# Kernel tuning notes

Measured on AMD Instinct MI355X. Metric: run time of the kernel, lower is better.

The kernel has to match this reference:

```python
import jax, jax.numpy as jnp
import numpy as np

EMBED_DIM = 1024
N_HEADS = 16
HEAD_DIM = EMBED_DIM // N_HEADS


def setup_inputs() -> dict:
    key = jax.random.key(0)
    ks = jax.random.split(key, 9)
    s = 1.0 / np.sqrt(EMBED_DIM)
    x = jax.random.normal(ks[0], (4, 2048, EMBED_DIM), dtype=jnp.float32)
    Wq = jax.random.uniform(ks[1], (EMBED_DIM, EMBED_DIM), jnp.float32, -s, s)
    bq = jax.random.uniform(ks[2], (EMBED_DIM,), jnp.float32, -s, s)
    Wk = jax.random.uniform(ks[3], (EMBED_DIM, EMBED_DIM), jnp.float32, -s, s)
    bk = jax.random.uniform(ks[4], (EMBED_DIM,), jnp.float32, -s, s)
    Wv = jax.random.uniform(ks[5], (EMBED_DIM, EMBED_DIM), jnp.float32, -s, s)
    bv = jax.random.uniform(ks[6], (EMBED_DIM,), jnp.float32, -s, s)
    Wo = jax.random.uniform(ks[7], (EMBED_DIM, EMBED_DIM), jnp.float32, -s, s)
    bo = jax.random.uniform(ks[8], (EMBED_DIM,), jnp.float32, -s, s)
    return {"x": x, "Wq": Wq, "bq": bq, "Wk": Wk, "bk": bk,
            "Wv": Wv, "bv": bv, "Wo": Wo, "bo": bo}


def reference(x, Wq, bq, Wk, bk, Wv, bv, Wo, bo):
    B, S, _ = x.shape
    # projections (PyTorch Linear: x @ W.T + b; weights stored as [in,out] here)
    q = x @ Wq + bq
    k = x @ Wk + bk
    v = x @ Wv + bv
    # [B, H, S, D]
    q = q.reshape(B, S, N_HEADS, HEAD_DIM).transpose(0, 2, 1, 3)
    k = k.reshape(B, S, N_HEADS, HEAD_DIM).transpose(0, 2, 1, 3)
    v = v.reshape(B, S, N_HEADS, HEAD_DIM).transpose(0, 2, 1, 3)
    scores = jnp.einsum('bhsd,bhtd->bhst', q, k) / np.sqrt(HEAD_DIM).astype(np.float32)
    attn = jax.nn.softmax(scores, axis=-1)
    out = jnp.einsum('bhst,bhtd->bhsd', attn, v)
    out = out.transpose(0, 2, 1, 3).reshape(B, S, EMBED_DIM)
    return out @ Wo + bo  # dropout=0 (eval) -> identity
```

## Files before the change

### kernel.cpp

```cpp
#include <hip/hip_runtime.h>
#include <stdint.h>

#define EMBED 1024
#define NH 16
#define HD 64
#define SEQ 2048
#define BATCH 4
#define M_TOT (BATCH*SEQ)
#define QSCALE 0.18033688011112042f

typedef __attribute__((ext_vector_type(8))) short short8;
typedef __attribute__((ext_vector_type(4))) float floatx4;
typedef __attribute__((ext_vector_type(4))) unsigned int uintx4;

__device__ __forceinline__ unsigned short f2bf(float f) {
    union { float f; unsigned int u; } v; v.f = f;
    unsigned int r = v.u + 0x7fffu + ((v.u >> 16) & 1u);
    return (unsigned short)(r >> 16);
}

__device__ __forceinline__ void load_lds16(const unsigned short* g, unsigned short* l) {
    __builtin_amdgcn_global_load_lds(
        (const __attribute__((address_space(1))) unsigned int*)g,
        (__attribute__((address_space(3))) unsigned int*)l, 16, 0, 0);
}

__global__ void cvt_x(const float* __restrict__ x, unsigned short* __restrict__ xb) {
    int i = (blockIdx.x * 256 + threadIdx.x) * 4;
    float4 v = *(const float4*)(x + i);
    ushort4 o;
    o.x = f2bf(v.x); o.y = f2bf(v.y); o.z = f2bf(v.z); o.w = f2bf(v.w);
    *(ushort4*)(xb + i) = o;
}

__global__ void wtrans(const float* __restrict__ w0, const float* __restrict__ w1,
                       const float* __restrict__ w2, const float* __restrict__ w3,
                       unsigned short* __restrict__ t0, unsigned short* __restrict__ t1,
                       unsigned short* __restrict__ t2, unsigned short* __restrict__ t3) {
    __shared__ float tile[32][33];
    const float* W; unsigned short* T;
    switch (blockIdx.z) { case 0: W=w0; T=t0; break; case 1: W=w1; T=t1; break;
                          case 2: W=w2; T=t2; break; default: W=w3; T=t3; }
    int n0 = blockIdx.x * 32, k0 = blockIdx.y * 32;
    int tx = threadIdx.x, ty = threadIdx.y;
    #pragma unroll
    for (int i = 0; i < 4; i++)
        tile[ty + i*8][tx] = W[(k0 + ty + i*8) * EMBED + n0 + tx];
    __syncthreads();
    #pragma unroll
    for (int i = 0; i < 4; i++)
        T[(n0 + ty + i*8) * EMBED + k0 + tx] = f2bf(tile[tx][ty + i*8]);
}

#define ST32(kt_) do { \
    const int b_ = (kt_) & 3; \
    const unsigned short* sa_ = Asrc + (kt_)*32; \
    const unsigned short* sb_ = Bsrc + (kt_)*32; \
    unsigned short* da_ = ldstA + b_*16384; \
    unsigned short* db_ = ldstB + b_*16384; \
    load_lds16(sa_,             da_); \
    load_lds16(sa_ + 128*EMBED, da_ + 4096); \
    load_lds16(sb_,             db_); \
    load_lds16(sb_ + 128*EMBED, db_ + 4096); \
  } while(0)

template<int WAITN, bool STG>
__device__ __forceinline__ void kt32(int t,
        const unsigned short* Abase, const unsigned short* Bbase,
        const unsigned short* Asrc, const unsigned short* Bsrc,
        unsigned short* ldstA, unsigned short* ldstB, floatx4 (&acc)[8][4]) {
    const int bo = (t & 3) * 16384;
    short8 fA[8], fB[4];
    #pragma unroll
    for (int m=0;m<8;m++) fA[m] = *(const short8*)(Abase + bo + m*512);
    #pragma unroll
    for (int n=0;n<4;n++) fB[n] = *(const short8*)(Bbase + bo + n*512);
    if (STG) ST32(t+3);
    #pragma unroll
    for (int m=0;m<8;m++)
      #pragma unroll
      for (int n=0;n<4;n++)
        acc[m][n] = __builtin_amdgcn_mfma_f32_16x16x32_bf16(fA[m], fB[n], acc[m][n], 0,0,0);
    if (WAITN >= 0) {
        asm volatile("s_waitcnt vmcnt(%0)" :: "i"(WAITN >= 0 ? WAITN : 0) : "memory");
        asm volatile("s_barrier" ::: "memory");
    }
}

template<int MODE>
__global__ __launch_bounds__(512, 2) void gemm32(
        const unsigned short* __restrict__ A, const unsigned short* __restrict__ BT,
        const float* __restrict__ b0, const float* __restrict__ b1, const float* __restrict__ b2,
        void* __restrict__ o0, void* __restrict__ o1, void* __restrict__ o2) {
    __shared__ unsigned short lds[4*16384];
    const int tid = threadIdx.x;
    const int lane = tid & 63, wave = tid >> 6;
    const int quad = lane >> 4, l16 = lane & 15;
    const int wm = wave >> 2, wn = wave & 3;
    const int id = blockIdx.x;
    const int xcd = id & 7, j = id >> 3;
    const int mblk = (xcd * 4 + (j & 3)) * 256;
    const int nblk = (j >> 2) * 256;

    const int srow = tid >> 2;
    const int scol = ((tid & 3) ^ (srow & 3)) * 8;
    const unsigned short* Asrc = A  + (size_t)(mblk + srow) * EMBED + scol;
    const unsigned short* Bsrc = BT + (size_t)(nblk + srow) * EMBED + scol;
    unsigned short* ldstA = lds + wave * 512;
    unsigned short* ldstB = lds + 8192 + wave * 512;

    const int cs = (quad ^ (l16 & 3)) * 8;
    const unsigned short* Abase = lds + (wm*128 + l16)*32 + cs;
    const unsigned short* Bbase = lds + 8192 + (wn*64 + l16)*32 + cs;

    floatx4 acc[8][4];
    #pragma unroll
    for (int m=0;m<8;m++)
      #pragma unroll
      for (int n=0;n<4;n++) acc[m][n] = (floatx4){0.f,0.f,0.f,0.f};

    ST32(0); ST32(1); ST32(2);
    asm volatile("s_waitcnt vmcnt(8)" ::: "memory");
    asm volatile("s_barrier" ::: "memory");

    #pragma unroll 4
    for (int t = 0; t < 28; ++t)
        kt32<8,true>(t, Abase, Bbase, Asrc, Bsrc, ldstA, ldstB, acc);
    kt32<8,true >(28, Abase, Bbase, Asrc, Bsrc, ldstA, ldstB, acc);
    kt32<4,false>(29, Abase, Bbase, Asrc, Bsrc, ldstA, ldstB, acc);
    kt32<0,false>(30, Abase, Bbase, Asrc, Bsrc, ldstA, ldstB, acc);
    kt32<-1,false>(31, Abase, Bbase, Asrc, Bsrc, ldstA, ldstB, acc);

    if (MODE == 1) {
        float* O = (float*)o0;
        #pragma unroll
        for (int mt=0;mt<8;mt++)
          #pragma unroll
          for (int nt=0;nt<4;nt++) {
            int col = nblk + wn*64 + nt*16 + l16;
            float bv = b0[col];
            #pragma unroll
            for (int r=0;r<4;r++) {
                int row = mblk + wm*128 + mt*16 + quad*4 + r;
                O[(size_t)row * EMBED + col] = acc[mt][nt][r] + bv;
            }
          }
    } else {
        int which = nblk >> 10;
        const float* bs = (which==0) ? b0 : (which==1) ? b1 : b2;
        if (which < 2) {
            unsigned short* O = (unsigned short*)((which==0) ? o0 : o1);
            float sc = (which==0) ? QSCALE : 1.f;
            #pragma unroll
            for (int mt=0;mt<8;mt++)
              #pragma unroll
              for (int nt=0;nt<4;nt++) {
                int coll = (nblk & 1023) + wn*64 + nt*16 + l16;
                float bv = bs[coll];
                int h = coll >> 6, d = coll & 63;
                #pragma unroll
                for (int r=0;r<4;r++) {
                    int row = mblk + wm*128 + mt*16 + quad*4 + r;
                    int b = row >> 11, s = row & 2047;
                    O[((size_t)(b*NH + h)*SEQ + s)*HD + d] = f2bf((acc[mt][nt][r] + bv) * sc);
                }
              }
        } else {
            unsigned short* T = lds;
            __syncthreads();
            #pragma unroll
            for (int nt=0;nt<4;nt++) {
                int cloc = wn*64 + nt*16 + l16;
                float bv = bs[(nblk & 1023) + cloc];
                int sw = (cloc & 3) << 3;
                #pragma unroll
                for (int mt=0;mt<8;mt++) {
                    int row0 = wm*128 + mt*16 + quad*4;
                    int sp0 = (row0 & ~31) | (((row0 >> 2) & 3) << 3) | (((row0 >> 4) & 1) << 2);
                    ushort4 w;
                    w.x = f2bf(acc[mt][nt][0] + bv);
                    w.y = f2bf(acc[mt][nt][1] + bv);
                    w.z = f2bf(acc[mt][nt][2] + bv);
                    w.w = f2bf(acc[mt][nt][3] + bv);
                    *(ushort4*)(T + cloc*256 + (sp0 ^ sw)) = w;
                }
            }
            __syncthreads();
            unsigned short* OV = (unsigned short*)o2;
            int s0 = (lane & 31) * 8, dloc = lane >> 5;
            size_t rowbase = ((size_t)((mblk >> 11)*1024 + (nblk & 1023))) * SEQ + (mblk & 2047);
            #pragma unroll
            for (int i=0;i<16;i++) {
                int c = wave*32 + i*2 + dloc;
                int sw2 = (c & 3) << 3;
                short8 v = *(const short8*)(T + c*256 + (s0 ^ sw2));
                *(short8*)(OV + rowbase + (size_t)c * SEQ + s0) = v;
            }
        }
    }
}

__global__ __launch_bounds__(512, 4) void attn(
    const unsigned short* __restrict__ Q, const unsigned short* __restrict__ K,
    const unsigned short* __restrict__ VTp, unsigned short* __restrict__ O) {
    __shared__ unsigned short kv[2][4096];
    unsigned short* kvf = &kv[0][0];
    int tid = threadIdx.x;
    int lane = tid & 63, wave = tid >> 6;
    int quad = lane >> 4, l16 = lane & 15;
    int id = blockIdx.x;
    int bh = (id & 7) * 8 + (id >> 6);
    int qblk = (id >> 3) & 7;
    int b = bh >> 4, h = bh & 15;
    int q0 = qblk * 256 + wave * 32;
    const unsigned short* Qb = Q + (size_t)bh * SEQ * HD;
    const unsigned short* Kb = K + (size_t)bh * SEQ * HD;
    const unsigned short* Vb = VTp + (size_t)bh * HD * SEQ;
    int li = (wave & 3) * 64 + lane;
    const unsigned short* src;
    int dstofs = (wave & 3) * 512 + ((wave >> 2) ? 2048 : 0);
    int src_step;
    if (wave < 4) {
        int t = li >> 3, slot = li & 7;
        int dblk = slot ^ (t & 7);
        src = Kb + (size_t)t * HD + dblk * 8;
        src_step = 32 * HD;
    } else {
        int d = li >> 2, slot = li & 3;
        int swz = (d & 3) ^ ((d >> 2) & 3);
        src = Vb + (size_t)d * SEQ + (slot ^ swz) * 8;
        src_step = 32;
    }
    short8 qf[2][2];
    #pragma unroll
    for (int mt=0;mt<2;mt++) {
        const unsigned short* qp = Qb + (size_t)(q0 + mt*16 + l16) * HD + quad*8;
        qf[mt][0] = *(const short8*)(qp);
        qf[mt][1] = *(const short8*)(qp + 32);
    }
    floatx4 o_acc[2][4], l_acc[2];
    #pragma unroll
    for (int mt=0;mt<2;mt++) {
        l_acc[mt] = (floatx4){0.f,0.f,0.f,0.f};
        #pragma unroll
        for (int dt=0;dt<4;dt++) o_acc[mt][dt] = (floatx4){0.f,0.f,0.f,0.f};
    }
    short8 ones;
    #pragma unroll
    for (int jj=0;jj<8;jj++) ones[jj] = (short)0x3F80;
    int koff[2][2], voff[4];
    #pragma unroll
    for (int nt=0;nt<2;nt++) {
        int t = nt*16 + l16;
        #pragma unroll
        for (int hh=0;hh<2;hh++)
            koff[nt][hh] = t*64 + ((hh*4 + quad) ^ (t & 7)) * 8;
    }
    #pragma unroll
    for (int dt=0;dt<4;dt++) {
        int d = dt*16 + l16;
        voff[dt] = 2048 + d*32 + ((quad ^ (d & 3) ^ ((d >> 2) & 3))) * 8;
    }

    load_lds16(src, kvf + dstofs);
    src += src_step;

    for (int it = 0; it < 64; ++it) {
        const unsigned short* kb = kvf + (it & 1) * 4096;
        if (it < 63) {
            load_lds16(src, kvf + ((it & 1) ^ 1) * 4096 + dstofs);
            src += src_step;
            asm volatile("s_waitcnt vmcnt(1)" ::: "memory");
        } else {
            asm volatile("s_waitcnt vmcnt(0)" ::: "memory");
        }
        __builtin_amdgcn_s_barrier();
        asm volatile("" ::: "memory");
        short8 kf[2][2], vf[4];
        #pragma unroll
        for (int nt=0;nt<2;nt++) {
            kf[nt][0] = *(const short8*)(kb + koff[nt][0]);
            kf[nt][1] = *(const short8*)(kb + koff[nt][1]);
        }
        #pragma unroll
        for (int dt=0;dt<4;dt++)
            vf[dt] = *(const short8*)(kb + voff[dt]);
        floatx4 sacc[2][2];
        __builtin_amdgcn_s_setprio(1);
        #pragma unroll
        for (int nt=0;nt<2;nt++)
          #pragma unroll
          for (int mt=0;mt<2;mt++) {
            floatx4 s = (floatx4){0.f,0.f,0.f,0.f};
            s = __builtin_amdgcn_mfma_f32_16x16x32_bf16(kf[nt][0], qf[mt][0], s, 0, 0, 0);
            s = __builtin_amdgcn_mfma_f32_16x16x32_bf16(kf[nt][1], qf[mt][1], s, 0, 0, 0);
            sacc[nt][mt] = s;
          }
        __builtin_amdgcn_s_setprio(0);
        short8 pf[2];
        #pragma unroll
        for (int mt=0;mt<2;mt++) {
            uintx4 pu;
            #pragma unroll
            for (int jp=0;jp<4;jp++) {
                int nt = jp >> 1, rp = (jp & 1) * 2;
                union { float f; unsigned int u; } e0, e1;
                e0.f = __builtin_amdgcn_exp2f(sacc[nt][mt][rp]);
                e1.f = __builtin_amdgcn_exp2f(sacc[nt][mt][rp+1]);
                pu[jp] = ((e1.u + 0x8000u) & 0xFFFF0000u) | ((e0.u + 0x8000u) >> 16);
            }
            pf[mt] = __builtin_bit_cast(short8, pu);
        }
        __builtin_amdgcn_s_setprio(1);
        #pragma unroll
        for (int mt=0;mt<2;mt++) {
            l_acc[mt] = __builtin_amdgcn_mfma_f32_16x16x32_bf16(ones, pf[mt], l_acc[mt], 0, 0, 0);
            #pragma unroll
            for (int dt=0;dt<4;dt++)
                o_acc[mt][dt] = __builtin_amdgcn_mfma_f32_16x16x32_bf16(vf[dt], pf[mt], o_acc[mt][dt], 0, 0, 0);
        }
        __builtin_amdgcn_s_setprio(0);
        asm volatile("" ::: "memory");
        __builtin_amdgcn_s_barrier();
    }
    #pragma unroll
    for (int mt=0;mt<2;mt++) {
        float inv = 1.f / l_acc[mt][0];
        int s = q0 + mt*16 + l16;
        #pragma unroll
        for (int dt=0;dt<4;dt++) {
            ushort4 w;
            w.x = f2bf(o_acc[mt][dt][0]*inv);
            w.y = f2bf(o_acc[mt][dt][1]*inv);
            w.z = f2bf(o_acc[mt][dt][2]*inv);
            w.w = f2bf(o_acc[mt][dt][3]*inv);
            *(ushort4*)(O + ((size_t)b*SEQ + s)*EMBED + h*HD + dt*16 + quad*4) = w;
        }
    }
}

extern "C" void kernel_launch(void* const* d_in, const int* in_sizes, int n_in,
                              void* d_out, int out_size, void* d_ws, size_t ws_size,
                              hipStream_t stream) {
    const float* x  = (const float*)d_in[0];
    const float* Wq = (const float*)d_in[1]; const float* bq = (const float*)d_in[2];
    const float* Wk = (const float*)d_in[3]; const float* bk = (const float*)d_in[4];
    const float* Wv = (const float*)d_in[5]; const float* bv = (const float*)d_in[6];
    const float* Wo = (const float*)d_in[7]; const float* bo = (const float*)d_in[8];
    char* ws = (char*)d_ws;
    unsigned short* xb  = (unsigned short*)(ws);
    unsigned short* WqT = (unsigned short*)(ws + (16ull<<20));
    unsigned short* WkT = (unsigned short*)(ws + (18ull<<20));
    unsigned short* WvT = (unsigned short*)(ws + (20ull<<20));
    unsigned short* WoT = (unsigned short*)(ws + (22ull<<20));
    unsigned short* Qb  = (unsigned short*)(ws + (24ull<<20));
    unsigned short* Kb  = (unsigned short*)(ws + (40ull<<20));
    unsigned short* VTb = (unsigned short*)(ws + (56ull<<20));
    unsigned short* Ob  = xb;

    cvt_x<<<(M_TOT*EMBED)/1024, 256, 0, stream>>>(x, xb);
    wtrans<<<dim3(32,32,4), dim3(32,8), 0, stream>>>(Wq,Wk,Wv,Wo, WqT,WkT,WvT,WoT);
    gemm32<0><<<dim3(384), 512, 0, stream>>>(xb, WqT, bq, bk, bv, Qb, Kb, VTb);
    attn<<<dim3(512), 512, 0, stream>>>(Qb, Kb, VTb, Ob);
    gemm32<1><<<dim3(128), 512, 0, stream>>>(Ob, WoT, bo, bo, bo, (float*)d_out, nullptr, nullptr);
}
```

Before: 267.7 us.

## Template GEMM on tile shape, switch to double buffering, retile output projection

Replaces the fixed 256x256 GEMM, which used a 4-stage LDS ring with 3-ahead prefetch, with a templated kernel using 2-stage double buffering and a full vmcnt(0) wait each k-step. This roughly halves LDS use so occupancy can rise (launch bound of 4 blocks per CU). The output projection now uses 128x128 tiles with 4 waves across 512 blocks instead of 128 large blocks, to fill the GPU better. The V-transpose epilogue is split into passes so it fits the smaller LDS. The risk is that the shallower prefetch exposes global-load latency, especially in the QKV GEMM, whose tiles are unchanged.

```diff
diff --git a/kernel.cpp b/kernel.cpp
--- a/kernel.cpp
+++ b/kernel.cpp
@@ -52,96 +52,88 @@
         T[(n0 + ty + i*8) * EMBED + k0 + tx] = f2bf(tile[tx][ty + i*8]);
 }
 
-#define ST32(kt_) do { \
-    const int b_ = (kt_) & 3; \
-    const unsigned short* sa_ = Asrc + (kt_)*32; \
-    const unsigned short* sb_ = Bsrc + (kt_)*32; \
-    unsigned short* da_ = ldstA + b_*16384; \
-    unsigned short* db_ = ldstB + b_*16384; \
-    load_lds16(sa_,             da_); \
-    load_lds16(sa_ + 128*EMBED, da_ + 4096); \
-    load_lds16(sb_,             db_); \
-    load_lds16(sb_ + 128*EMBED, db_ + 4096); \
-  } while(0)
-
-template<int WAITN, bool STG>
-__device__ __forceinline__ void kt32(int t,
-        const unsigned short* Abase, const unsigned short* Bbase,
-        const unsigned short* Asrc, const unsigned short* Bsrc,
-        unsigned short* ldstA, unsigned short* ldstB, floatx4 (&acc)[8][4]) {
-    const int bo = (t & 3) * 16384;
-    short8 fA[8], fB[4];
-    #pragma unroll
-    for (int m=0;m<8;m++) fA[m] = *(const short8*)(Abase + bo + m*512);
-    #pragma unroll
-    for (int n=0;n<4;n++) fB[n] = *(const short8*)(Bbase + bo + n*512);
-    if (STG) ST32(t+3);
-    #pragma unroll
-    for (int m=0;m<8;m++)
-      #pragma unroll
-      for (int n=0;n<4;n++)
-        acc[m][n] = __builtin_amdgcn_mfma_f32_16x16x32_bf16(fA[m], fB[n], acc[m][n], 0,0,0);
-    if (WAITN >= 0) {
-        asm volatile("s_waitcnt vmcnt(%0)" :: "i"(WAITN >= 0 ? WAITN : 0) : "memory");
-        asm volatile("s_barrier" ::: "memory");
-    }
-}
-
-template<int MODE>
-__global__ __launch_bounds__(512, 2) void gemm32(
+template<int MODE, int BM, int BN, int NW>
+__global__ __launch_bounds__(NW*64, 4) void gemmk(
         const unsigned short* __restrict__ A, const unsigned short* __restrict__ BT,
         const float* __restrict__ b0, const float* __restrict__ b1, const float* __restrict__ b2,
         void* __restrict__ o0, void* __restrict__ o1, void* __restrict__ o2) {
-    __shared__ unsigned short lds[4*16384];
+    constexpr int THREADS = NW*64;
+    constexpr int WC = NW/2;
+    constexpr int WMT = BM/2, WNT = BN/WC;
+    constexpr int FM = WMT/16, FN = WNT/16;
+    constexpr int RPI = THREADS/4;
+    constexpr int BUFS = (BM+BN)*32;
+    static_assert(BM == 2*RPI && BN == 2*RPI, "staging assumes 2 issues/operand");
+    __shared__ unsigned short lds[2*BUFS];
     const int tid = threadIdx.x;
     const int lane = tid & 63, wave = tid >> 6;
     const int quad = lane >> 4, l16 = lane & 15;
-    const int wm = wave >> 2, wn = wave & 3;
+    const int wm = wave / WC, wn = wave % WC;
     const int id = blockIdx.x;
+    constexpr int MS = (M_TOT/BM)/8;
     const int xcd = id & 7, j = id >> 3;
-    const int mblk = (xcd * 4 + (j & 3)) * 256;
-    const int nblk = (j >> 2) * 256;
+    const int mblk = (xcd * MS + (j % MS)) * BM;
+    const int nblk = (j / MS) * BN;
 
     const int srow = tid >> 2;
     const int scol = ((tid & 3) ^ (srow & 3)) * 8;
     const unsigned short* Asrc = A  + (size_t)(mblk + srow) * EMBED + scol;
     const unsigned short* Bsrc = BT + (size_t)(nblk + srow) * EMBED + scol;
-    unsigned short* ldstA = lds + wave * 512;
-    unsigned short* ldstB = lds + 8192 + wave * 512;
+    unsigned short* sda = lds + wave * 512;
+    unsigned short* sdb = lds + BM*32 + wave * 512;
 
     const int cs = (quad ^ (l16 & 3)) * 8;
-    const unsigned short* Abase = lds + (wm*128 + l16)*32 + cs;
-    const unsigned short* Bbase = lds + 8192 + (wn*64 + l16)*32 + cs;
-
-    floatx4 acc[8][4];
-    #pragma unroll
-    for (int m=0;m<8;m++)
+    const unsigned short* Abase = lds + (wm*WMT + l16)*32 + cs;
+    const unsigned short* Bbase = lds + BM*32 + (wn*WNT + l16)*32 + cs;
+
+    floatx4 acc[FM][FN];
+    #pragma unroll
+    for (int m=0;m<FM;m++)
       #pragma unroll
-      for (int n=0;n<4;n++) acc[m][n] = (floatx4){0.f,0.f,0.f,0.f};
-
-    ST32(0); ST32(1); ST32(2);
-    asm volatile("s_waitcnt vmcnt(8)" ::: "memory");
+      for (int n=0;n<FN;n++) acc[m][n] = (floatx4){0.f,0.f,0.f,0.f};
+
+#define ST(t_) do { \
+    const int buf_ = (t_) & 1; const int ko_ = (t_)*32; \
+    load_lds16(Asrc + ko_,              sda + buf_*BUFS); \
+    load_lds16(Asrc + ko_ + RPI*EMBED,  sda + buf_*BUFS + RPI*32); \
+    load_lds16(Bsrc + ko_,              sdb + buf_*BUFS); \
+    load_lds16(Bsrc + ko_ + RPI*EMBED,  sdb + buf_*BUFS + RPI*32); \
+  } while(0)
+
+    ST(0);
+    asm volatile("s_waitcnt vmcnt(0)" ::: "memory");
     asm volatile("s_barrier" ::: "memory");
 
-    #pragma unroll 4
-    for (int t = 0; t < 28; ++t)
-        kt32<8,true>(t, Abase, Bbase, Asrc, Bsrc, ldstA, ldstB, acc);
-    kt32<8,true >(28, Abase, Bbase, Asrc, Bsrc, ldstA, ldstB, acc);
-    kt32<4,false>(29, Abase, Bbase, Asrc, Bsrc, ldstA, ldstB, acc);
-    kt32<0,false>(30, Abase, Bbase, Asrc, Bsrc, ldstA, ldstB, acc);
-    kt32<-1,false>(31, Abase, Bbase, Asrc, Bsrc, ldstA, ldstB, acc);
-
-    if (MODE == 1) {
+    #pragma unroll 2
+    for (int t = 0; t < 32; ++t) {
+        const int bo = (t & 1) * BUFS;
+        short8 fA[FM], fB[FN];
+        #pragma unroll
+        for (int m=0;m<FM;m++) fA[m] = *(const short8*)(Abase + bo + m*512);
+        #pragma unroll
+        for (int n=0;n<FN;n++) fB[n] = *(const short8*)(Bbase + bo + n*512);
+        if (t < 31) ST(t+1);
+        #pragma unroll
+        for (int m=0;m<FM;m++)
+          #pragma unroll
+          for (int n=0;n<FN;n++)
+            acc[m][n] = __builtin_amdgcn_mfma_f32_16x16x32_bf16(fA[m], fB[n], acc[m][n], 0,0,0);
+        if (t < 31) asm volatile("s_waitcnt vmcnt(0)" ::: "memory");
+        asm volatile("s_barrier" ::: "memory");
+    }
+#undef ST
+
+    if constexpr (MODE == 1) {
         float* O = (float*)o0;
         #pragma unroll
-        for (int mt=0;mt<8;mt++)
+        for (int mt=0;mt<FM;mt++)
           #pragma unroll
-          for (int nt=0;nt<4;nt++) {
-            int col = nblk + wn*64 + nt*16 + l16;
+          for (int nt=0;nt<FN;nt++) {
+            int col = nblk + wn*WNT + nt*16 + l16;
             float bv = b0[col];
             #pragma unroll
             for (int r=0;r<4;r++) {
-                int row = mblk + wm*128 + mt*16 + quad*4 + r;
+                int row = mblk + wm*WMT + mt*16 + quad*4 + r;
                 O[(size_t)row * EMBED + col] = acc[mt][nt][r] + bv;
             }
           }
@@ -152,49 +144,55 @@
             unsigned short* O = (unsigned short*)((which==0) ? o0 : o1);
             float sc = (which==0) ? QSCALE : 1.f;
             #pragma unroll
-            for (int mt=0;mt<8;mt++)
+            for (int mt=0;mt<FM;mt++)
               #pragma unroll
-              for (int nt=0;nt<4;nt++) {
-                int coll = (nblk & 1023) + wn*64 + nt*16 + l16;
+              for (int nt=0;nt<FN;nt++) {
+                int coll = (nblk & 1023) + wn*WNT + nt*16 + l16;
                 float bv = bs[coll];
                 int h = coll >> 6, d = coll & 63;
                 #pragma unroll
                 for (int r=0;r<4;r++) {
-                    int row = mblk + wm*128 + mt*16 + quad*4 + r;
+                    int row = mblk + wm*WMT + mt*16 + quad*4 + r;
                     int b = row >> 11, s = row & 2047;
                     O[((size_t)(b*NH + h)*SEQ + s)*HD + d] = f2bf((acc[mt][nt][r] + bv) * sc);
                 }
               }
         } else {
             unsigned short* T = lds;
+            unsigned short* OV = (unsigned short*)o2;
+            size_t rowbase = ((size_t)((mblk >> 11)*1024 + (nblk & 1023))) * SEQ + (mblk & 2047);
             __syncthreads();
             #pragma unroll
-            for (int nt=0;nt<4;nt++) {
-                int cloc = wn*64 + nt*16 + l16;
-                float bv = bs[(nblk & 1023) + cloc];
-                int sw = (cloc & 3) << 3;
+            for (int p = 0; p < BN/128; ++p) {
+                if ((wn >> 1) == p) {
+                    #pragma unroll
+                    for (int nt=0;nt<FN;nt++) {
+                        int cloc = wn*WNT + nt*16 + l16;
+                        float bv = bs[(nblk & 1023) + cloc];
+                        int sw = (cloc & 3) << 3;
+                        #pragma unroll
+                        for (int mt=0;mt<FM;mt++) {
+                            int row0 = wm*WMT + mt*16 + quad*4;
+                            int sp0 = (row0 & ~31) | (((row0 >> 2) & 3) << 3) | (((row0 >> 4) & 1) << 2);
+                            ushort4 w;
+                            w.x = f2bf(acc[mt][nt][0] + bv);
+                            w.y = f2bf(acc[mt][nt][1] + bv);
+                            w.z = f2bf(acc[mt][nt][2] + bv);
+                            w.w = f2bf(acc[mt][nt][3] + bv);
+                            *(ushort4*)(T + (cloc & 127)*256 + (sp0 ^ sw)) = w;
+                        }
+                    }
+                }
+                __syncthreads();
+                int s0 = (lane & 31) * 8, dloc = lane >> 5;
                 #pragma unroll
-                for (int mt=0;mt<8;mt++) {
-                    int row0 = wm*128 + mt*16 + quad*4;
-                    int sp0 = (row0 & ~31) | (((row0 >> 2) & 3) << 3) | (((row0 >> 4) & 1) << 2);
-                    ushort4 w;
-                    w.x = f2bf(acc[mt][nt][0] + bv);
-                    w.y = f2bf(acc[mt][nt][1] + bv);
-                    w.z = f2bf(acc[mt][nt][2] + bv);
-                    w.w = f2bf(acc[mt][nt][3] + bv);
-                    *(ushort4*)(T + cloc*256 + (sp0 ^ sw)) = w;
+                for (int i=0;i<128/(NW*2);i++) {
+                    int cl = wave*(128/NW) + i*2 + dloc;
+                    int sw2 = (cl & 3) << 3;
+                    short8 v = *(const short8*)(T + cl*256 + (s0 ^ sw2));
+                    *(short8*)(OV + rowbase + (size_t)(p*128 + cl) * SEQ + s0) = v;
                 }
-            }
-            __syncthreads();
-            unsigned short* OV = (unsigned short*)o2;
-            int s0 = (lane & 31) * 8, dloc = lane >> 5;
-            size_t rowbase = ((size_t)((mblk >> 11)*1024 + (nblk & 1023))) * SEQ + (mblk & 2047);
-            #pragma unroll
-            for (int i=0;i<16;i++) {
-                int c = wave*32 + i*2 + dloc;
-                int sw2 = (c & 3) << 3;
-                short8 v = *(const short8*)(T + c*256 + (s0 ^ sw2));
-                *(short8*)(OV + rowbase + (size_t)c * SEQ + s0) = v;
+                __syncthreads();
             }
         }
     }
@@ -360,7 +358,7 @@
 
     cvt_x<<<(M_TOT*EMBED)/1024, 256, 0, stream>>>(x, xb);
     wtrans<<<dim3(32,32,4), dim3(32,8), 0, stream>>>(Wq,Wk,Wv,Wo, WqT,WkT,WvT,WoT);
-    gemm32<0><<<dim3(384), 512, 0, stream>>>(xb, WqT, bq, bk, bv, Qb, Kb, VTb);
+    gemmk<0,256,256,8><<<dim3(384), 512, 0, stream>>>(xb, WqT, bq, bk, bv, Qb, Kb, VTb);
     attn<<<dim3(512), 512, 0, stream>>>(Qb, Kb, VTb, Ob);
-    gemm32<1><<<dim3(128), 512, 0, stream>>>(Ob, WoT, bo, bo, bo, (float*)d_out, nullptr, nullptr);
-}
+    gemmk<1,128,128,4><<<dim3(512), 256, 0, stream>>>(Ob, WoT, bo, bo, bo, (float*)d_out, nullptr, nullptr);
+}
```

Result: slower. 672.5 us (+151.2%).
